# Kernel optimization log

Measured on AMD Instinct MI355X. Metric: run time of the kernel, lower is better.

Reference implementation:

```python
import jax, jax.numpy as jnp
import numpy as np

B, S, H, T = 64, 512, 768, 50


def setup_inputs() -> dict:
    key = jax.random.key(0)
    k1, k2, k3, k4, k5, k6, k7 = jax.random.split(key, 7)
    full_hidden = jax.random.normal(k1, (B, S, H), dtype=jnp.float32)
    tag_ids = jax.random.randint(k2, (B, S), 0, T)
    lengths = jax.random.randint(k3, (B,), 1, S + 1)
    mask = (jnp.arange(S)[None, :] < lengths[:, None])  # valid-prefix mask, t=0 always on
    W = jax.random.normal(k4, (H, T), dtype=jnp.float32) * 0.02
    b = jnp.zeros((T,), dtype=jnp.float32)
    start_transitions = jax.random.normal(k5, (T,), dtype=jnp.float32) * 0.1
    end_transitions = jax.random.normal(k6, (T,), dtype=jnp.float32) * 0.1
    transitions = jax.random.normal(k7, (T, T), dtype=jnp.float32) * 0.1
    return {
        'full_hidden': full_hidden, 'W': W, 'b': b,
        'start_transitions': start_transitions, 'end_transitions': end_transitions,
        'transitions': transitions, 'tag_ids': tag_ids, 'mask': mask,
    }


def _crf_losses(emissions, start_transitions, end_transitions, transitions, tag_ids, mask):
    # emissions: [B,S,T]; returns per-sequence loss = log_partition - gold_score (pytorch-crf, reduction='none', negated)
    maskf = mask.astype(emissions.dtype)
    Bn = tag_ids.shape[0]
    bidx = jnp.arange(Bn)
    # ---- numerator: score of the gold tag path ----
    em_tag = jnp.take_along_axis(emissions, tag_ids[..., None], axis=2)[..., 0]  # [B,S]
    num = start_transitions[tag_ids[:, 0]] + em_tag[:, 0]
    trans_score = transitions[tag_ids[:, :-1], tag_ids[:, 1:]]  # [B,S-1]
    num = num + jnp.sum((trans_score + em_tag[:, 1:]) * maskf[:, 1:], axis=1)
    lengths = jnp.sum(mask.astype(jnp.int32), axis=1)
    last_tags = tag_ids[bidx, lengths - 1]
    num = num + end_transitions[last_tags]
    # ---- denominator: log partition via forward DP (scan over time) ----
    alpha0 = start_transitions[None, :] + emissions[:, 0]  # [B,T]

    def step(alpha, inp):
        em_t, m_t = inp  # [B,T], [B]
        nxt = jax.nn.logsumexp(alpha[:, :, None] + transitions[None, :, :] + em_t[:, None, :], axis=1)
        alpha = jnp.where(m_t[:, None], nxt, alpha)
        return alpha, None

    em_rest = jnp.swapaxes(emissions[:, 1:], 0, 1)  # [S-1,B,T]
    m_rest = jnp.swapaxes(mask[:, 1:], 0, 1)        # [S-1,B]
    alpha, _ = jax.lax.scan(step, alpha0, (em_rest, m_rest))
    den = jax.nn.logsumexp(alpha + end_transitions[None, :], axis=1)
    return den - num  # [B]


def reference(full_hidden, W, b, start_transitions, end_transitions, transitions, tag_ids, mask):
    # dropout is identity in eval mode (config dropout applied at train time only)
    emissions = jnp.einsum('bsh,ht->bst', full_hidden, W) + b  # hid2tag
    return _crf_losses(emissions, start_transitions, end_transitions, transitions, tag_ids, mask)
```

## Files before the change

### kernel.cpp

```cpp
#include <hip/hip_runtime.h>
#include <cstdint>
#include <cstddef>

#define Bn 64
#define Sn 512
#define Hn 768
#define Tn 50
#define CH 32
#define NCH 16
#define EP 52

typedef short short8 __attribute__((ext_vector_type(8)));
typedef float floatx4 __attribute__((ext_vector_type(4)));

__device__ __forceinline__ uint32_t rne_bf16(float x) {
  uint32_t u = __float_as_uint(x);
  return (u + 0x7FFFu + ((u >> 16) & 1u)) >> 16;
}
__device__ __forceinline__ uint32_t pack2(float a, float b) {
  return rne_bf16(a) | (rne_bf16(b) << 16);
}
__device__ __forceinline__ float rdlane(float v, int i) {
  return __uint_as_float(__builtin_amdgcn_readlane(__float_as_uint(v), i));
}

__global__ __launch_bounds__(256) void prep_kernel(
    const float* __restrict__ W, const float* __restrict__ trans,
    const int* __restrict__ mask, uint32_t* __restrict__ wfrag,
    int* __restrict__ lenbuf, float* __restrict__ Ee,
    float* __restrict__ EeT) {
  const int blk = blockIdx.x;
  const int tid = threadIdx.x;
  if (blk < 64) {
    if (tid < 64) {
      int s = 0;
      for (int t = tid; t < Sn; t += 64) s += mask[blk * Sn + t];
#pragma unroll
      for (int off = 1; off < 64; off <<= 1) s += __shfl_xor(s, off);
      if (tid == 0) lenbuf[blk] = s;
    }
    return;
  }
  if (blk == 88) {
    for (int gid = tid; gid < Tn * Tn; gid += 256) {
      const int r = gid / Tn, cl = gid - r * Tn;
      const float v = __expf(trans[gid]);
      Ee[r * EP + cl] = v;
      EeT[cl * EP + r] = v;
    }
    return;
  }
  const int gid = (blk - 64) * 256 + tid;
  const int f = gid >> 6;
  const int l = gid & 63;
  const int ks = f >> 2, nt = f & 3;
  const int col = nt * 16 + (l & 15);
  const int k0 = ks * 32 + (l >> 4) * 8;
  float v[8];
#pragma unroll
  for (int j = 0; j < 8; ++j)
    v[j] = (col < Tn) ? W[(size_t)(k0 + j) * Tn + col] : 0.f;
  uint4 d;
  d.x = pack2(v[0], v[1]);
  d.y = pack2(v[2], v[3]);
  d.z = pack2(v[4], v[5]);
  d.w = pack2(v[6], v[7]);
  ((uint4*)wfrag)[gid] = d;
}

#define BK 64
__global__ __launch_bounds__(256, 2) void emissions_kernel(
    const float* __restrict__ hidden, const uint32_t* __restrict__ wfrag,
    const float* __restrict__ bias, const int* __restrict__ lenbuf,
    float* __restrict__ em) {
  const int blk = blockIdx.x;
  const int bb = blk >> 3, cc = blk & 7;
  if (cc * 64 >= lenbuf[bb]) return;
  const int tid = threadIdx.x;
  const int lane = tid & 63;
  const int w = tid >> 6;
  const int g = lane >> 4;
  const int li = lane & 15;
  const int row0 = blk * 64;
  __shared__ char lds_raw[64 * 128];

  floatx4 acc[4];
#pragma unroll
  for (int nt = 0; nt < 4; ++nt) acc[nt] = (floatx4)0.f;

  const float* hbase = hidden + (size_t)row0 * Hn;
  const short8* wf = (const short8*)wfrag;

#define LOADCH(dst, ch)                                                      \
  _Pragma("unroll") for (int k = 0; k < 4; ++k) dst[k] =                     \
      *(const float4*)(hbase + (size_t)(w * 16 + 4 * k + g) * Hn + (ch)*BK + \
                       li * 4);
#define WRITELDS(src)                                                        \
  _Pragma("unroll") for (int k = 0; k < 4; ++k) {                            \
    const int r = w * 16 + 4 * k + g;                                        \
    const uint32_t b0 = pack2(src[k].x, src[k].y);                           \
    const uint32_t b1 = pack2(src[k].z, src[k].w);                           \
    const int byteoff = r * 128 + ((li * 8) ^ ((r & 7) << 4));               \
    *(uint2*)(lds_raw + byteoff) = make_uint2(b0, b1);                       \
  }
#define COMPUTE(ch)                                                          \
  _Pragma("unroll") for (int ks = 0; ks < 2; ++ks) {                         \
    const int r = w * 16 + li;                                               \
    const int kb = ks * 64 + g * 16;                                         \
    const short8 af =                                                        \
        *(const short8*)(lds_raw + r * 128 + (kb ^ ((r & 7) << 4)));         \
    const int ksg = (ch)*2 + ks;                                             \
    _Pragma("unroll") for (int nt = 0; nt < 4; ++nt) {                       \
      const short8 bf = wf[(ksg * 4 + nt) * 64 + lane];                      \
      acc[nt] =                                                              \
          __builtin_amdgcn_mfma_f32_16x16x32_bf16(af, bf, acc[nt], 0, 0, 0); \
    }                                                                        \
  }

  float4 pfA[4], pfB[4];
  LOADCH(pfA, 0)
  LOADCH(pfB, 1)
#pragma unroll
  for (int chp = 0; chp < Hn / BK / 2; ++chp) {
    const int ch = 2 * chp;
    WRITELDS(pfA)
    if (ch + 2 < Hn / BK) LOADCH(pfA, ch + 2)
    COMPUTE(ch)
    WRITELDS(pfB)
    if (ch + 3 < Hn / BK) LOADCH(pfB, ch + 3)
    COMPUTE(ch + 1)
  }
#undef LOADCH
#undef WRITELDS
#undef COMPUTE

#pragma unroll
  for (int nt = 0; nt < 4; ++nt) {
    const int col = nt * 16 + li;
    if (col < Tn) {
      const float bs = bias[col];
#pragma unroll
      for (int r = 0; r < 4; ++r) {
        const int row = row0 + w * 16 + g * 4 + r;
        em[(size_t)row * Tn + col] = acc[nt][r] + bs;
      }
    }
  }
}

__global__ __launch_bounds__(64, 1) void scan_kernel(
    const float* __restrict__ em, const float* __restrict__ startT,
    const float* __restrict__ trans, const float* __restrict__ Ee,
    const float* __restrict__ EeT, const int* __restrict__ tag,
    const int* __restrict__ lenbuf, float* __restrict__ fvec,
    float* __restrict__ gvec, float* __restrict__ Lf,
    float* __restrict__ numpart) {
  const int blk = blockIdx.x;
  const int b = blk >> 5;
  const int c = (blk >> 1) & (NCH - 1);
  const int dir = blk & 1;
  const int len = lenbuf[b];
  const int t0 = 1 + c * CH;
  if (t0 >= len) return;
  if (dir && c == 0) return;
  const int t1 = (t0 + CH < len) ? t0 + CH : len;
  const int L = t1 - t0;
  const int lane = threadIdx.x;
  const int jc = lane < Tn ? lane : 0;
  const bool live = lane < Tn;
  const float* emb = em + (size_t)b * Sn * Tn;

  if (!dir) {
    float npv = 0.f;
    if (lane < L) {
      const int t = t0 + lane;
      const int tp = tag[b * Sn + t - 1], tc = tag[b * Sn + t];
      npv = trans[tp * Tn + tc] + emb[(size_t)t * Tn + tc];
    }
#pragma unroll
    for (int off = 1; off < 64; off <<= 1) npv += __shfl_xor(npv, off);
    if (lane == 0) numpart[b * NCH + c] = npv;
  }

  const float* ebase = (dir ? Ee : EeT) + jc * EP;
  float e[Tn];
#pragma unroll
  for (int i = 0; i < Tn; ++i) e[i] = ebase[i];

  float Cacc = 0.f;
  float q;
  if (!dir)
    q = live ? (c == 0 ? __expf(startT[jc] + emb[jc]) : 1.f) : 0.f;
  else
    q = live ? 1.f : 0.f;

#define T_OF(k) (dir ? (t1 - 1 - (k)) : (t0 + (k)))
  float ld1 = emb[(size_t)T_OF(0) * Tn + jc];
  const float ld2 = emb[(size_t)T_OF(L > 1 ? 1 : 0) * Tn + jc];
  float ee = live ? __expf(ld1) : 0.f;
  ld1 = ld2;

  for (int k = 0; k < L; ++k) {
    const float ee_cur = ee;
    const int kn = (k + 2 < L) ? k + 2 : L - 1;
    const float ldn = emb[(size_t)T_OF(kn) * Tn + jc];
    ee = live ? __expf(ld1) : 0.f;
    ld1 = ldn;

    const float x = dir ? ee_cur * q : q;
    float s0 = 0.f, s1 = 0.f, s2 = 0.f, s3 = 0.f;
#pragma unroll
    for (int i = 0; i < 48; i += 4) {
      s0 = fmaf(rdlane(x, i + 0), e[i + 0], s0);
      s1 = fmaf(rdlane(x, i + 1), e[i + 1], s1);
      s2 = fmaf(rdlane(x, i + 2), e[i + 2], s2);
      s3 = fmaf(rdlane(x, i + 3), e[i + 3], s3);
    }
    s0 = fmaf(rdlane(x, 48), e[48], s0);
    s1 = fmaf(rdlane(x, 49), e[49], s1);
    const float s = (s0 + s1) + (s2 + s3);
    q = dir ? s : ee_cur * s;

    if ((k & 7) == 7) {
      float M = q;
#pragma unroll
      for (int off = 1; off < 64; off <<= 1) M = fmaxf(M, __shfl_xor(M, off));
      const float r = __builtin_amdgcn_rcpf(M);
      q *= r;
      Cacc -= __logf(r);
    }
  }
#undef T_OF

  float M = q;
#pragma unroll
  for (int off = 1; off < 64; off <<= 1) M = fmaxf(M, __shfl_xor(M, off));
  const float r = __builtin_amdgcn_rcpf(M);
  const float qn = live ? q * r : 0.f;
  Cacc -= __logf(r);
  if (dir) {
    gvec[((size_t)b * NCH + c) * 64 + lane] = qn;
  } else {
    fvec[((size_t)b * NCH + c) * 64 + lane] = qn;
    if (lane == 0) Lf[b * NCH + c] = Cacc;
  }
}

__global__ __launch_bounds__(64) void stitch_kernel(
    const float* __restrict__ em, const float* __restrict__ startT,
    const float* __restrict__ endT, const int* __restrict__ tag,
    const int* __restrict__ lenbuf, const float* __restrict__ fvec,
    const float* __restrict__ gvec, const float* __restrict__ Lf,
    const float* __restrict__ numpart, float* __restrict__ out) {
  const int b = blockIdx.x;
  const int lane = threadIdx.x;
  const int len = lenbuf[b];
  const int C = (len - 1 + CH - 1) / CH;
  const int jc = lane < Tn ? lane : 0;
  const bool live = lane < Tn;
  const float* emb = em + (size_t)b * Sn * Tn;

  float np = (lane < C) ? numpart[b * NCH + lane] : 0.f;
#pragma unroll
  for (int off = 1; off < 64; off <<= 1) np += __shfl_xor(np, off);
  const int tg0 = tag[b * Sn];
  const int tgl = tag[b * Sn + len - 1];
  np += startT[tg0] + emb[tg0] + endT[tgl];

  float den;
  if (C == 0) {
    float v = live ? (startT[jc] + emb[jc] + endT[jc]) : -INFINITY;
    float M = v;
#pragma unroll
    for (int off = 1; off < 64; off <<= 1) M = fmaxf(M, __shfl_xor(M, off));
    float s = __expf(v - M);
#pragma unroll
    for (int off = 1; off < 64; off <<= 1) s += __shfl_xor(s, off);
    den = M + __logf(s);
  } else {
    const float ev = live ? __expf(endT[jc]) : 0.f;
    float d = fvec[((size_t)b * NCH + C - 1) * 64 + lane] * ev;
#pragma unroll
    for (int off = 1; off < 64; off <<= 1) d += __shfl_xor(d, off);
    den = Lf[b * NCH + C - 1] + __logf(d);
    for (int c2 = 1; c2 < C; ++c2) {
      const float g = gvec[((size_t)b * NCH + c2) * 64 + lane];
      const float f = fvec[((size_t)b * NCH + c2 - 1) * 64 + lane];
      float dot = g * f;
      float gs = g;
#pragma unroll
      for (int off = 1; off < 64; off <<= 1) {
        dot += __shfl_xor(dot, off);
        gs += __shfl_xor(gs, off);
      }
      den += Lf[b * NCH + c2 - 1] + __logf(dot) - __logf(gs);
    }
  }
  if (lane == 0) out[b] = den - np;
}

extern "C" void kernel_launch(void* const* d_in, const int* in_sizes, int n_in,
                              void* d_out, int out_size, void* d_ws,
                              size_t ws_size, hipStream_t stream) {
  const float* hidden = (const float*)d_in[0];
  const float* W = (const float*)d_in[1];
  const float* bias = (const float*)d_in[2];
  const float* startT = (const float*)d_in[3];
  const float* endT = (const float*)d_in[4];
  const float* trans = (const float*)d_in[5];
  const int* tag = (const int*)d_in[6];
  const int* mask = (const int*)d_in[7];
  float* out = (float*)d_out;

  char* ws = (char*)d_ws;
  float* em = (float*)ws;
  uint32_t* wfrag = (uint32_t*)(ws + 6553600);
  int* lenbuf = (int*)(ws + 6651904);
  float* Ee = (float*)(ws + 6652160);
  float* EeT = (float*)(ws + 6662976);
  float* fvec = (float*)(ws + 6673792);
  float* gvec = (float*)(ws + 6935936);
  float* Lf = (float*)(ws + 7198080);
  float* numpart = (float*)(ws + 7202176);

  prep_kernel<<<89, 256, 0, stream>>>(W, trans, mask, wfrag, lenbuf, Ee, EeT);
  emissions_kernel<<<(Bn * Sn) / 64, 256, 0, stream>>>(hidden, wfrag, bias,
                                                       lenbuf, em);
  scan_kernel<<<Bn * NCH * 2, 64, 0, stream>>>(em, startT, trans, Ee, EeT, tag,
                                               lenbuf, fvec, gvec, Lf, numpart);
  stitch_kernel<<<Bn, 64, 0, stream>>>(em, startT, endT, tag, lenbuf, fvec,
                                       gvec, Lf, numpart, out);
}
```

Measured before the change: 61.72 us.

## Halve CRF scan chunk length, coalesce transition matrix loads, relax emissions occupancy

```diff
diff --git a/kernel.cpp b/kernel.cpp
--- a/kernel.cpp
+++ b/kernel.cpp
@@ -6,9 +6,8 @@
 #define Sn 512
 #define Hn 768
 #define Tn 50
-#define CH 32
-#define NCH 16
-#define EP 52
+#define CH 16
+#define NCH 32
 
 typedef short short8 __attribute__((ext_vector_type(8)));
 typedef float floatx4 __attribute__((ext_vector_type(4)));
@@ -27,8 +26,8 @@
 __global__ __launch_bounds__(256) void prep_kernel(
     const float* __restrict__ W, const float* __restrict__ trans,
     const int* __restrict__ mask, uint32_t* __restrict__ wfrag,
-    int* __restrict__ lenbuf, float* __restrict__ Ee,
-    float* __restrict__ EeT) {
+    int* __restrict__ lenbuf, float* __restrict__ EfwdP,
+    float* __restrict__ EbwdP) {
   const int blk = blockIdx.x;
   const int tid = threadIdx.x;
   if (blk < 64) {
@@ -42,11 +41,10 @@
     return;
   }
   if (blk == 88) {
-    for (int gid = tid; gid < Tn * Tn; gid += 256) {
-      const int r = gid / Tn, cl = gid - r * Tn;
-      const float v = __expf(trans[gid]);
-      Ee[r * EP + cl] = v;
-      EeT[cl * EP + r] = v;
+    for (int gid = tid; gid < Tn * 64; gid += 256) {
+      const int i = gid >> 6, j = gid & 63;
+      EfwdP[gid] = (j < Tn) ? __expf(trans[i * Tn + j]) : 0.f;
+      EbwdP[gid] = (j < Tn) ? __expf(trans[j * Tn + i]) : 0.f;
     }
     return;
   }
@@ -69,7 +67,7 @@
 }
 
 #define BK 64
-__global__ __launch_bounds__(256, 2) void emissions_kernel(
+__global__ __launch_bounds__(256, 1) void emissions_kernel(
     const float* __restrict__ hidden, const uint32_t* __restrict__ wfrag,
     const float* __restrict__ bias, const int* __restrict__ lenbuf,
     float* __restrict__ em) {
@@ -150,13 +148,13 @@
 
 __global__ __launch_bounds__(64, 1) void scan_kernel(
     const float* __restrict__ em, const float* __restrict__ startT,
-    const float* __restrict__ trans, const float* __restrict__ Ee,
-    const float* __restrict__ EeT, const int* __restrict__ tag,
+    const float* __restrict__ trans, const float* __restrict__ EfwdP,
+    const float* __restrict__ EbwdP, const int* __restrict__ tag,
     const int* __restrict__ lenbuf, float* __restrict__ fvec,
     float* __restrict__ gvec, float* __restrict__ Lf,
     float* __restrict__ numpart) {
   const int blk = blockIdx.x;
-  const int b = blk >> 5;
+  const int b = blk >> 6;
   const int c = (blk >> 1) & (NCH - 1);
   const int dir = blk & 1;
   const int len = lenbuf[b];
@@ -182,10 +180,10 @@
     if (lane == 0) numpart[b * NCH + c] = npv;
   }
 
-  const float* ebase = (dir ? Ee : EeT) + jc * EP;
+  const float* ebase = dir ? EbwdP : EfwdP;
   float e[Tn];
 #pragma unroll
-  for (int i = 0; i < Tn; ++i) e[i] = ebase[i];
+  for (int i = 0; i < Tn; ++i) e[i] = ebase[i * 64 + jc];
 
   float Cacc = 0.f;
   float q;
@@ -316,18 +314,20 @@
   float* em = (float*)ws;
   uint32_t* wfrag = (uint32_t*)(ws + 6553600);
   int* lenbuf = (int*)(ws + 6651904);
-  float* Ee = (float*)(ws + 6652160);
-  float* EeT = (float*)(ws + 6662976);
-  float* fvec = (float*)(ws + 6673792);
-  float* gvec = (float*)(ws + 6935936);
-  float* Lf = (float*)(ws + 7198080);
-  float* numpart = (float*)(ws + 7202176);
-
-  prep_kernel<<<89, 256, 0, stream>>>(W, trans, mask, wfrag, lenbuf, Ee, EeT);
+  float* EfwdP = (float*)(ws + 6652160);
+  float* EbwdP = (float*)(ws + 6664960);
+  float* fvec = (float*)(ws + 6677760);
+  float* gvec = (float*)(ws + 7202048);
+  float* Lf = (float*)(ws + 7726336);
+  float* numpart = (float*)(ws + 7734528);
+
+  prep_kernel<<<89, 256, 0, stream>>>(W, trans, mask, wfrag, lenbuf, EfwdP,
+                                      EbwdP);
   emissions_kernel<<<(Bn * Sn) / 64, 256, 0, stream>>>(hidden, wfrag, bias,
                                                        lenbuf, em);
-  scan_kernel<<<Bn * NCH * 2, 64, 0, stream>>>(em, startT, trans, Ee, EeT, tag,
-                                               lenbuf, fvec, gvec, Lf, numpart);
+  scan_kernel<<<Bn * NCH * 2, 64, 0, stream>>>(em, startT, trans, EfwdP, EbwdP,
+                                               tag, lenbuf, fvec, gvec, Lf,
+                                               numpart);
   stitch_kernel<<<Bn, 64, 0, stream>>>(em, startT, endT, tag, lenbuf, fvec,
                                        gvec, Lf, numpart, out);
 }
```

Result: no change. 61.24 us (-0.8%).
